# Kernel optimization log

Hardware: AMD Instinct MI355X
Metric: run time of the kernel (lower is better)

## Reference

```python
import jax, jax.numpy as jnp
import numpy as np

H, HS, NH, T = 2048, 64, 32, 1024
DD, DA, DG, DV = 64, 64, 128, 32


def _ln(x, w, b, eps):
    mu = x.mean(-1, keepdims=True)
    var = ((x - mu) ** 2).mean(-1, keepdims=True)
    return (x - mu) / jnp.sqrt(var + eps) * w + b


def setup_inputs() -> dict:
    key = jax.random.key(0)
    ks = jax.random.split(key, 40)
    n = lambda i, shape, s=0.02: (jax.random.normal(ks[i], shape, jnp.float32) * s)
    u = lambda i, shape: jax.random.uniform(ks[i], shape, jnp.float32)
    return {
        'x': jax.random.normal(ks[0], (1, T, H), jnp.float32),
        'state1': jax.random.normal(ks[1], (1, H), jnp.float32),
        'state2': jnp.zeros((NH, HS, HS), jnp.float32),
        'v_first': jax.random.normal(ks[2], (1, T, H), jnp.float32),
        'x_r': u(3, (H,)), 'x_w': u(4, (H,)), 'x_k': u(5, (H,)),
        'x_v': u(6, (H,)), 'x_a': u(7, (H,)), 'x_g': u(8, (H,)),
        'W_r': n(9, (H, H)), 'W_k': n(10, (H, H)), 'W_v': n(11, (H, H)), 'W_o': n(12, (H, H)),
        'w0': n(13, (H,), 0.5) - 0.6,
        'w1': n(14, (H, DD)), 'w2': n(15, (DD, H)),
        'a0': jnp.zeros((H,), jnp.float32), 'a1': n(16, (H, DA)), 'a2': n(17, (DA, H)),
        'v0': jnp.zeros((H,), jnp.float32), 'v1': n(18, (H, DV)), 'v2': n(19, (DV, H)),
        'g1': n(20, (H, DG)), 'g2': n(21, (DG, H)),
        'k_k': n(22, (NH, HS), 0.5) + 1.0, 'k_a': n(23, (NH, HS), 0.5) + 1.0,
        'r_k': n(24, (NH, HS), 0.5),
        'ln_x_w': jnp.ones((H,), jnp.float32), 'ln_x_b': jnp.zeros((H,), jnp.float32),
        'ln1_w': jnp.ones((H,), jnp.float32), 'ln1_b': jnp.zeros((H,), jnp.float32),
    }


def reference(x, state1, state2, v_first, x_r, x_w, x_k, x_v, x_a, x_g,
              W_r, W_k, W_v, W_o, w0, w1, w2, a0, a1, a2, v0, v1, v2,
              g1, g2, k_k, k_a, r_k, ln_x_w, ln_x_b, ln1_w, ln1_b):
    T = x.shape[1]
    NH, HS = k_k.shape
    Hd = NH * HS
    last_x = x
    xn = _ln(x, ln1_w, ln1_b, 1e-5)
    # token shift: sx = shifted_past - x
    past = jnp.concatenate([state1[:, None, :], xn[:, :-1, :]], axis=1)
    sx = past - xn
    state1_out = xn[:, -1, :]
    xr = xn + x_r * sx
    xw = xn + x_w * sx
    xk = xn + x_k * sx
    xv = xn + x_v * sx
    xa = xn + x_a * sx
    xg = xn + x_g * sx
    r = xr @ W_r.T                                  # [1,T,H]
    k = (xk @ W_k.T).reshape(T, NH, HS)
    v = xv @ W_v.T                                  # [1,T,H]
    g = jax.nn.sigmoid(xg @ g1) @ g2                # gate
    a = jax.nn.sigmoid(a0 + (xa @ a1) @ a2).reshape(T, NH, HS)
    w = jnp.tanh(xw @ w1) @ w2                      # decay LoRA
    kk = k * k_k
    kk = kk / (jnp.linalg.norm(kk, axis=-1, keepdims=True) + 1e-12)
    k = k * (1.0 + (a - 1.0) * k_a)
    # layer_id != 0: v residual toward v_first
    v = v + (v_first - v) * jax.nn.sigmoid(v0 + (xv @ v1) @ v2)
    w = jnp.exp(-0.606531 * jax.nn.sigmoid(w0 + w)).reshape(T, NH, HS)
    b_seq = kk * a        # in-context addition direction
    a_seq = -kk           # removal direction
    r3 = r.reshape(T, NH, HS)
    v3 = v.reshape(T, NH, HS)

    def step(S, ts):
        w_t, k_t, v_t, a_t, b_t, r_t = ts          # each [NH,HS]
        S = S * w_t[:, None, :]                     # column-wise decay
        sa = jnp.einsum('hij,hj->hi', S, a_t)       # S @ a
        S = S + sa[:, :, None] * b_t[:, None, :] + v_t[:, :, None] * k_t[:, None, :]
        out = jnp.einsum('hij,hj->hi', S, r_t)      # S @ r
        return S, out

    state2_out, y = jax.lax.scan(step, state2, (w, k, v3, a_seq, b_seq, r3))  # y: [T,NH,HS]
    y = _ln(y, 1.0, 0.0, 0.00064)                   # GroupNorm-style per-head LN (no affine)
    y = y.reshape(1, T, Hd) * ln_x_w + ln_x_b
    bonus = ((r3 * k * r_k).sum(-1, keepdims=True) * v3).reshape(1, T, Hd)
    y = (y + bonus) * g
    y = y @ W_o.T
    return (last_x + y, state1_out, state2_out, v_first)
```

## Files before the change

### kernel.cpp

```cpp
#include <hip/hip_runtime.h>
#include <hip/hip_bf16.h>
#include <cstdint>
#include <cstddef>

#define T_TOK 1024
#define H_DIM 2048
#define NH 32
#define HS 64
#define TH (T_TOK * H_DIM)
#define HH (H_DIM * H_DIM)

using short8 = __attribute__((ext_vector_type(8))) short;
using f32x4  = __attribute__((ext_vector_type(4))) float;
typedef __hip_bfloat16 bf16;

__device__ __forceinline__ float sigmoidf_(float x) { return 1.0f / (1.0f + expf(-x)); }

__device__ __forceinline__ float wsum64(float v) {
#pragma unroll
    for (int m = 32; m; m >>= 1) v += __shfl_xor(v, m, 64);
    return v;
}

__device__ __forceinline__ float dpp_add16(float x) {
    int t;
    t = __builtin_amdgcn_update_dpp(0, __float_as_int(x), 0xB1, 0xF, 0xF, true);
    x += __int_as_float(t);
    t = __builtin_amdgcn_update_dpp(0, __float_as_int(x), 0x4E, 0xF, 0xF, true);
    x += __int_as_float(t);
    t = __builtin_amdgcn_update_dpp(0, __float_as_int(x), 0x141, 0xF, 0xF, true);
    x += __int_as_float(t);
    t = __builtin_amdgcn_update_dpp(0, __float_as_int(x), 0x140, 0xF, 0xF, true);
    x += __int_as_float(t);
    return x;
}

struct CastPar { const float* src[4]; bf16* dst[4]; };
__global__ __launch_bounds__(256) void castw_kernel(CastPar p) {
    int z = blockIdx.z;
    const float4* s = (const float4*)p.src[z];
    bf16* d = p.dst[z];
    int i = blockIdx.x * 256 + threadIdx.x;
    float4 v = s[i];
    int b = i * 4;
    d[b + 0] = __float2bfloat16(v.x);
    d[b + 1] = __float2bfloat16(v.y);
    d[b + 2] = __float2bfloat16(v.z);
    d[b + 3] = __float2bfloat16(v.w);
}

struct TPar { const float* src[8]; bf16* dst[8]; int R[8]; int C[8]; };
__global__ __launch_bounds__(256) void transpose_kernel(TPar p) {
    int z = blockIdx.z;
    int R = p.R[z], C = p.C[z];
    int e = blockIdx.x * 256 + threadIdx.x;
    if (e >= R * C) return;
    int r = e / C, c = e % C;
    p.dst[z][(size_t)c * R + r] = __float2bfloat16(p.src[z][e]);
}

__global__ __launch_bounds__(256) void ln_kernel(const float* __restrict__ x,
                                                 const float* __restrict__ w,
                                                 const float* __restrict__ b,
                                                 float* __restrict__ xn,
                                                 float* __restrict__ s1out) {
    int t = blockIdx.x, tid = threadIdx.x;
    const float* xt = x + (size_t)t * H_DIM;
    float v[8]; float s = 0.f, s2 = 0.f;
#pragma unroll
    for (int e = 0; e < 8; e++) { v[e] = xt[tid + 256 * e]; s += v[e]; s2 += v[e] * v[e]; }
    s = wsum64(s); s2 = wsum64(s2);
    __shared__ float ls[8];
    int wid = tid >> 6, ln = tid & 63;
    if (ln == 0) { ls[wid] = s; ls[4 + wid] = s2; }
    __syncthreads();
    s = ls[0] + ls[1] + ls[2] + ls[3];
    s2 = ls[4] + ls[5] + ls[6] + ls[7];
    float mu = s * (1.f / H_DIM);
    float var = s2 * (1.f / H_DIM) - mu * mu;
    float inv = rsqrtf(var + 1e-5f);
#pragma unroll
    for (int e = 0; e < 8; e++) {
        int h = tid + 256 * e;
        float o = (v[e] - mu) * inv * w[h] + b[h];
        xn[(size_t)t * H_DIM + h] = o;
        if (t == T_TOK - 1) s1out[h] = o;
    }
}

struct MixPar { const float* xn; const float* state1; const float* mv[6]; bf16* out[6]; };
__global__ __launch_bounds__(256) void mix_kernel(MixPar p) {
    int t = blockIdx.x, tid = threadIdx.x;
#pragma unroll
    for (int e = 0; e < 8; e++) {
        int h = tid + 256 * e;
        size_t idx = (size_t)t * H_DIM + h;
        float cur = p.xn[idx];
        float prev = (t == 0) ? p.state1[h] : p.xn[idx - H_DIM];
        float sx = prev - cur;
#pragma unroll
        for (int q = 0; q < 6; q++)
            p.out[q][idx] = __float2bfloat16(cur + p.mv[q][h] * sx);
    }
}

typedef const __attribute__((address_space(1))) uint32_t* gp1_t;
typedef __attribute__((address_space(3))) uint32_t* lp3_t;
__device__ __forceinline__ void async16(const bf16* g, short* l) {
    __builtin_amdgcn_global_load_lds((gp1_t)g, (lp3_t)l, 16, 0, 0);
}

struct BGPar { const bf16* X[4]; const bf16* W[4]; float* out[4]; const float* resid[4]; };
__global__ __launch_bounds__(256) void bgemm_kernel(BGPar p) {
    int z = blockIdx.z;
    const bf16* __restrict__ X = p.X[z];
    const bf16* __restrict__ W = p.W[z];
    float* __restrict__ out = p.out[z];
    const float* __restrict__ resid = p.resid[z];

    __shared__ short As[4][128 * 32];
    __shared__ short Bs[4][128 * 32];

    int m0 = blockIdx.y * 128, n0 = blockIdx.x * 128;
    int tid = threadIdx.x, lane = tid & 63, wv = tid >> 6;
    int m_off = (wv >> 1) * 64, n_off = (wv & 1) * 64;
    int lr = lane & 15, lq = lane >> 4;

    int srow = lane >> 2;
    int scol = (lane & 3) * 8;
    const bf16* Ag0 = X + (size_t)(m0 + wv * 32 + srow) * 2048 + scol;
    const bf16* Ag1 = Ag0 + (size_t)16 * 2048;
    const bf16* Bg0 = W + (size_t)(n0 + wv * 32 + srow) * 2048 + scol;
    const bf16* Bg1 = Bg0 + (size_t)16 * 2048;

    auto issue = [&](int at, int nb) {
        int kk = at * 32;
        async16(Ag0 + kk, &As[nb][(wv * 32) * 32]);
        async16(Ag1 + kk, &As[nb][(wv * 32 + 16) * 32]);
        async16(Bg0 + kk, &Bs[nb][(wv * 32) * 32]);
        async16(Bg1 + kk, &Bs[nb][(wv * 32 + 16) * 32]);
    };

    f32x4 acc[4][4];
#pragma unroll
    for (int a = 0; a < 4; a++)
#pragma unroll
        for (int b = 0; b < 4; b++)
#pragma unroll
            for (int r = 0; r < 4; r++) acc[a][b][r] = 0.f;

    issue(0, 0); issue(1, 1); issue(2, 2);

    for (int it = 0; it < 64; it++) {
        int nt = it + 3;
        int at = nt > 63 ? 63 : nt;
        issue(at, nt & 3);
        asm volatile("s_waitcnt vmcnt(12)" ::: "memory");
        asm volatile("s_barrier" ::: "memory");
        int buf = it & 3;
        short8 af[4], bfr[4];
#pragma unroll
        for (int mi = 0; mi < 4; mi++)
            af[mi] = *(const short8*)&As[buf][(m_off + mi * 16 + lr) * 32 + lq * 8];
#pragma unroll
        for (int ni = 0; ni < 4; ni++)
            bfr[ni] = *(const short8*)&Bs[buf][(n_off + ni * 16 + lr) * 32 + lq * 8];
#pragma unroll
        for (int mi = 0; mi < 4; mi++)
#pragma unroll
            for (int ni = 0; ni < 4; ni++)
                acc[mi][ni] = __builtin_amdgcn_mfma_f32_16x16x32_bf16(af[mi], bfr[ni], acc[mi][ni], 0, 0, 0);
        asm volatile("s_barrier" ::: "memory");
    }
    asm volatile("s_waitcnt vmcnt(0)" ::: "memory");

#pragma unroll
    for (int mi = 0; mi < 4; mi++)
#pragma unroll
        for (int ni = 0; ni < 4; ni++)
#pragma unroll
            for (int r = 0; r < 4; r++) {
                int rowg = m0 + m_off + mi * 16 + lq * 4 + r;
                int colg = n0 + n_off + ni * 16 + lr;
                size_t o = (size_t)rowg * 2048 + colg;
                float v = acc[mi][ni][r];
                if (resid) v += resid[o];
                out[o] = v;
            }
}

#define BM 128
#define BN 128
#define BK 32
#define LDK 40

__device__ __forceinline__ void gemm_core(const bf16* __restrict__ X, const bf16* __restrict__ W,
                                          int M, int N, int K, int act,
                                          const float* __restrict__ bias,
                                          float* __restrict__ outF, bf16* __restrict__ outB) {
    __shared__ short As[BM * LDK];
    __shared__ short Bs[BN * LDK];
    int m0 = blockIdx.y * BM, n0 = blockIdx.x * BN;
    if (n0 >= N) return;
    int tid = threadIdx.x;
    int lane = tid & 63, wid = tid >> 6;
    int m_off = (wid >> 1) * 64, n_off = (wid & 1) * 64;
    int lr = lane & 15, lq = lane >> 4;

    f32x4 acc[4][4];
#pragma unroll
    for (int a = 0; a < 4; a++)
#pragma unroll
        for (int b = 0; b < 4; b++)
#pragma unroll
            for (int r = 0; r < 4; r++) acc[a][b][r] = 0.f;

    for (int k0 = 0; k0 < K; k0 += BK) {
#pragma unroll
        for (int it = 0; it < 2; it++) {
            int c = tid + it * 256;
            int r = c >> 2;
            int cc = (c & 3) * 8;
            uint4 va = *(const uint4*)(X + (size_t)(m0 + r) * K + k0 + cc);
            *(uint4*)&As[r * LDK + cc] = va;
            uint4 vb;
            if (n0 + r < N) vb = *(const uint4*)(W + (size_t)(n0 + r) * K + k0 + cc);
            else            vb = make_uint4(0u, 0u, 0u, 0u);
            *(uint4*)&Bs[r * LDK + cc] = vb;
        }
        __syncthreads();
        short8 af[4], bfr[4];
#pragma unroll
        for (int mi = 0; mi < 4; mi++)
            af[mi] = *(const short8*)&As[(m_off + mi * 16 + lr) * LDK + lq * 8];
#pragma unroll
        for (int ni = 0; ni < 4; ni++)
            bfr[ni] = *(const short8*)&Bs[(n_off + ni * 16 + lr) * LDK + lq * 8];
#pragma unroll
        for (int mi = 0; mi < 4; mi++)
#pragma unroll
            for (int ni = 0; ni < 4; ni++)
                acc[mi][ni] = __builtin_amdgcn_mfma_f32_16x16x32_bf16(af[mi], bfr[ni], acc[mi][ni], 0, 0, 0);
        __syncthreads();
    }
#pragma unroll
    for (int mi = 0; mi < 4; mi++)
#pragma unroll
        for (int ni = 0; ni < 4; ni++)
#pragma unroll
            for (int r = 0; r < 4; r++) {
                int rowg = m0 + m_off + mi * 16 + lq * 4 + r;
                int colg = n0 + n_off + ni * 16 + lr;
                if (colg < N) {
                    float v = acc[mi][ni][r];
                    if (bias) v += bias[colg];
                    if (act == 1) v = sigmoidf_(v);
                    else if (act == 2) v = tanhf(v);
                    size_t o = (size_t)rowg * N + colg;
                    if (outF) outF[o] = v;
                    else      outB[o] = __float2bfloat16(v);
                }
            }
}

struct GPar {
    const bf16* X[4]; const bf16* W[4];
    float* outF[4]; bf16* outB[4];
    const float* bias[4];
    int N[4]; int K[4]; int act[4]; int M;
};
__global__ __launch_bounds__(256) void gemm_z_kernel(GPar p) {
    int z = blockIdx.z;
    gemm_core(p.X[z], p.W[z], p.M, p.N[z], p.K[z], p.act[z], p.bias[z], p.outF[z], p.outB[z]);
}

__global__ __launch_bounds__(64) void prep_kernel(float* __restrict__ k_io, float* __restrict__ v_io,
                                                  const float* __restrict__ v_first,
                                                  const float* __restrict__ vres,
                                                  float* __restrict__ w_io, float* __restrict__ a_io,
                                                  float* __restrict__ as_out,
                                                  const float* __restrict__ k_k,
                                                  const float* __restrict__ k_a,
                                                  const float* __restrict__ w0) {
    int h = blockIdx.x, t = blockIdx.y, i = threadIdx.x;
    int hi = h * HS + i;
    size_t idx = (size_t)t * H_DIM + hi;
    float kf = k_io[idx];
    float kk = kf * k_k[hi];
    float ss = wsum64(kk * kk);
    float kkn = kk / (sqrtf(ss) + 1e-12f);
    float a = a_io[idx];
    k_io[idx] = kf * (1.f + (a - 1.f) * k_a[hi]);
    float vv = v_io[idx];
    v_io[idx] = vv + (v_first[idx] - vv) * vres[idx];
    w_io[idx] = expf(-0.606531f * sigmoidf_(w0[hi] + w_io[idx]));
    a_io[idx] = kkn * a;
    as_out[idx] = -kkn;
}

struct SlotV { f32x4 w, a, b, k, r; float v; };

#define SCAN_ISSUE(sl, tt)                                                              \
    do {                                                                                \
        int tc_ = (tt) < T_TOK ? (tt) : T_TOK - 1;                                      \
        const float* wp_ = w_s + (size_t)tc_ * H_DIM + hb;                              \
        const float* ap_ = as_s + (size_t)tc_ * H_DIM + hb;                             \
        const float* bp_ = b_s + (size_t)tc_ * H_DIM + hb;                              \
        const float* kp_ = k_s + (size_t)tc_ * H_DIM + hb;                              \
        const float* rp_ = r_s + (size_t)tc_ * H_DIM + hb;                              \
        const float* vp_ = v_s + (size_t)tc_ * H_DIM + hb;                              \
        asm volatile("global_load_dwordx4 %0, %1, %2" : "=v"((sl).w) : "v"(jow), "s"(wp_)); \
        asm volatile("global_load_dwordx4 %0, %1, %2" : "=v"((sl).a) : "v"(jow), "s"(ap_)); \
        asm volatile("global_load_dwordx4 %0, %1, %2" : "=v"((sl).b) : "v"(jow), "s"(bp_)); \
        asm volatile("global_load_dwordx4 %0, %1, %2" : "=v"((sl).k) : "v"(jow), "s"(kp_)); \
        asm volatile("global_load_dwordx4 %0, %1, %2" : "=v"((sl).r) : "v"(jow), "s"(rp_)); \
        asm volatile("global_load_dword %0, %1, %2" : "=v"((sl).v) : "v"(rowoff), "s"(vp_)); \
    } while (0)

#define SCAN_PIN(sl)                                                                    \
    asm volatile("" : "+v"((sl).w), "+v"((sl).a), "+v"((sl).b), "+v"((sl).k),           \
                      "+v"((sl).r), "+v"((sl).v))

__device__ __forceinline__ void scan_compute(float S[4], const SlotV& s,
                                             const float* __restrict__ yp, int rowoff) {
    float sa = 0.f;
#pragma unroll
    for (int e = 0; e < 4; e++) { S[e] *= s.w[e]; sa = fmaf(S[e], s.a[e], sa); }
    sa = dpp_add16(sa);
    float o = 0.f;
#pragma unroll
    for (int e = 0; e < 4; e++) {
        S[e] = fmaf(sa, s.b[e], fmaf(s.v, s.k[e], S[e]));
        o = fmaf(S[e], s.r[e], o);
    }
    o = dpp_add16(o);
    asm volatile("global_store_dword %0, %1, %2" :: "v"(rowoff), "v"(o), "s"(yp) : "memory");
}

#define SCAN_STEP(d, t, W)                                                              \
    do {                                                                                \
        asm volatile("s_waitcnt vmcnt(" W ")");                                         \
        SCAN_PIN(sv[d]);                                                                \
        scan_compute(S, sv[d], y + (size_t)(t) * H_DIM + hb, rowoff);                   \
        SCAN_ISSUE(sv[d], (t) + 4);                                                     \
    } while (0)

__global__ __launch_bounds__(64) void scan_kernel(const float* __restrict__ w_s,
                                                  const float* __restrict__ k_s,
                                                  const float* __restrict__ v_s,
                                                  const float* __restrict__ as_s,
                                                  const float* __restrict__ b_s,
                                                  const float* __restrict__ r_s,
                                                  const float* __restrict__ s2in,
                                                  float* __restrict__ y,
                                                  float* __restrict__ s2out) {
    int h = blockIdx.x, q = blockIdx.y;
    int lane = threadIdx.x;
    int il = lane >> 4, jb = lane & 15;
    int row = q * 4 + il;
    int jo = jb * 4;
    int hb = h * HS;
    int jow = jo * 4;
    int rowoff = row * 4;

    float S[4];
    {
        const float* s0 = s2in + (size_t)h * HS * HS + (size_t)row * HS + jo;
        float4 t0 = *(const float4*)s0;
        S[0] = t0.x; S[1] = t0.y; S[2] = t0.z; S[3] = t0.w;
    }

    SlotV sv[4];
    SCAN_ISSUE(sv[0], 0);
    SCAN_ISSUE(sv[1], 1);
    SCAN_ISSUE(sv[2], 2);
    SCAN_ISSUE(sv[3], 3);

    SCAN_STEP(0, 0, "18");
    SCAN_STEP(1, 1, "19");
    SCAN_STEP(2, 2, "20");
    SCAN_STEP(3, 3, "21");
    for (int tb = 4; tb < T_TOK; tb += 4) {
        SCAN_STEP(0, tb + 0, "21");
        SCAN_STEP(1, tb + 1, "21");
        SCAN_STEP(2, tb + 2, "21");
        SCAN_STEP(3, tb + 3, "21");
    }
    asm volatile("s_waitcnt vmcnt(0)" ::: "memory");

    {
        float* so = s2out + (size_t)h * HS * HS + (size_t)row * HS + jo;
        float4 t0;
        t0.x = S[0]; t0.y = S[1]; t0.z = S[2]; t0.w = S[3];
        *(float4*)so = t0;
    }
}

__global__ __launch_bounds__(64) void post_kernel(const float* __restrict__ y,
                                                  const float* __restrict__ r_s,
                                                  const float* __restrict__ k_s,
                                                  const float* __restrict__ v_s,
                                                  const float* __restrict__ g_s,
                                                  const float* __restrict__ r_k,
                                                  const float* __restrict__ lnw,
                                                  const float* __restrict__ lnb,
                                                  bf16* __restrict__ ybig) {
    int h = blockIdx.x, t = blockIdx.y, i = threadIdx.x;
    int hi = h * HS + i;
    size_t idx = (size_t)t * H_DIM + hi;
    float yv = y[idx];
    float mu = wsum64(yv) * (1.f / HS);
    float d = yv - mu;
    float var = wsum64(d * d) * (1.f / HS);
    float yn = d * rsqrtf(var + 0.00064f);
    float bd = wsum64(r_s[idx] * k_s[idx] * r_k[hi]);
    float val = (yn * lnw[hi] + lnb[hi] + bd * v_s[idx]) * g_s[idx];
    ybig[idx] = __float2bfloat16(val);
}

extern "C" void kernel_launch(void* const* d_in, const int* in_sizes, int n_in,
                              void* d_out, int out_size, void* d_ws, size_t ws_size,
                              hipStream_t stream) {
    const float* x      = (const float*)d_in[0];
    const float* state1 = (const float*)d_in[1];
    const float* state2 = (const float*)d_in[2];
    const float* vfirst = (const float*)d_in[3];
    const float* x_r = (const float*)d_in[4];
    const float* x_w = (const float*)d_in[5];
    const float* x_k = (const float*)d_in[6];
    const float* x_v = (const float*)d_in[7];
    const float* x_a = (const float*)d_in[8];
    const float* x_g = (const float*)d_in[9];
    const float* W_r = (const float*)d_in[10];
    const float* W_k = (const float*)d_in[11];
    const float* W_v = (const float*)d_in[12];
    const float* W_o = (const float*)d_in[13];
    const float* w0 = (const float*)d_in[14];
    const float* w1 = (const float*)d_in[15];
    const float* w2 = (const float*)d_in[16];
    const float* a0 = (const float*)d_in[17];
    const float* a1 = (const float*)d_in[18];
    const float* a2 = (const float*)d_in[19];
    const float* v0 = (const float*)d_in[20];
    const float* v1 = (const float*)d_in[21];
    const float* v2 = (const float*)d_in[22];
    const float* g1 = (const float*)d_in[23];
    const float* g2 = (const float*)d_in[24];
    const float* k_k = (const float*)d_in[25];
    const float* k_a = (const float*)d_in[26];
    const float* r_k = (const float*)d_in[27];
    const float* ln_x_w = (const float*)d_in[28];
    const float* ln_x_b = (const float*)d_in[29];
    const float* ln1_w = (const float*)d_in[30];
    const float* ln1_b = (const float*)d_in[31];

    float* out0 = (float*)d_out;
    float* out1 = out0 + TH;
    float* out2 = out1 + H_DIM;
    float* out3 = out2 + NH * HS * HS;

    float* F = (float*)d_ws;
    float* xn   = F;
    float* as_s = F;
    float* rb   = F + (size_t)1 * TH;
    float* kb   = F + (size_t)2 * TH;
    float* vb   = F + (size_t)3 * TH;
    float* ab   = F + (size_t)4 * TH;
    float* wpre = F + (size_t)5 * TH;
    float* vresb= F + (size_t)6 * TH;
    float* gb   = F + (size_t)7 * TH;
    float* yb   = F + (size_t)8 * TH;
    bf16* B = (bf16*)(F + (size_t)9 * TH);
    bf16 *xrb = B, *xwb = B + (size_t)TH, *xkb = B + (size_t)2 * TH,
         *xvb = B + (size_t)3 * TH, *xab = B + (size_t)4 * TH, *xgb = B + (size_t)5 * TH;
    bf16* Wrb = B + (size_t)6 * TH;
    bf16* Wkb = Wrb + (size_t)HH;
    bf16* Wvb = Wkb + (size_t)HH;
    bf16* Wob = Wvb + (size_t)HH;
    bf16* pp = Wob + (size_t)HH;
    bf16* a1T = pp; pp += (size_t)H_DIM * 64;
    bf16* w1T = pp; pp += (size_t)H_DIM * 64;
    bf16* v1T = pp; pp += (size_t)H_DIM * 32;
    bf16* g1T = pp; pp += (size_t)H_DIM * 128;
    bf16* a2T = pp; pp += (size_t)H_DIM * 64;
    bf16* w2T = pp; pp += (size_t)H_DIM * 64;
    bf16* v2T = pp; pp += (size_t)H_DIM * 32;
    bf16* g2T = pp; pp += (size_t)H_DIM * 128;
    bf16* amid = pp; pp += (size_t)T_TOK * 64;
    bf16* wmid = pp; pp += (size_t)T_TOK * 64;
    bf16* vmid = pp; pp += (size_t)T_TOK * 32;
    bf16* gmid = pp; pp += (size_t)T_TOK * 128;
    bf16* ybig = pp; pp += (size_t)TH;

    CastPar cp;
    cp.src[0] = W_r; cp.src[1] = W_k; cp.src[2] = W_v; cp.src[3] = W_o;
    cp.dst[0] = Wrb; cp.dst[1] = Wkb; cp.dst[2] = Wvb; cp.dst[3] = Wob;
    castw_kernel<<<dim3(HH / 4 / 256, 1, 4), 256, 0, stream>>>(cp);

    TPar tp;
    tp.src[0] = a1; tp.dst[0] = a1T; tp.R[0] = H_DIM; tp.C[0] = 64;
    tp.src[1] = w1; tp.dst[1] = w1T; tp.R[1] = H_DIM; tp.C[1] = 64;
    tp.src[2] = v1; tp.dst[2] = v1T; tp.R[2] = H_DIM; tp.C[2] = 32;
    tp.src[3] = g1; tp.dst[3] = g1T; tp.R[3] = H_DIM; tp.C[3] = 128;
    tp.src[4] = a2; tp.dst[4] = a2T; tp.R[4] = 64;  tp.C[4] = H_DIM;
    tp.src[5] = w2; tp.dst[5] = w2T; tp.R[5] = 64;  tp.C[5] = H_DIM;
    tp.src[6] = v2; tp.dst[6] = v2T; tp.R[6] = 32;  tp.C[6] = H_DIM;
    tp.src[7] = g2; tp.dst[7] = g2T; tp.R[7] = 128; tp.C[7] = H_DIM;
    transpose_kernel<<<dim3((H_DIM * 128 + 255) / 256, 1, 8), 256, 0, stream>>>(tp);

    ln_kernel<<<dim3(T_TOK), 256, 0, stream>>>(x, ln1_w, ln1_b, xn, out1);

    MixPar mp; mp.xn = xn; mp.state1 = state1;
    mp.mv[0] = x_r; mp.mv[1] = x_w; mp.mv[2] = x_k; mp.mv[3] = x_v; mp.mv[4] = x_a; mp.mv[5] = x_g;
    mp.out[0] = xrb; mp.out[1] = xwb; mp.out[2] = xkb; mp.out[3] = xvb; mp.out[4] = xab; mp.out[5] = xgb;
    mix_kernel<<<dim3(T_TOK), 256, 0, stream>>>(mp);

    BGPar bp{};
    bp.X[0] = xrb; bp.W[0] = Wrb; bp.out[0] = rb; bp.resid[0] = nullptr;
    bp.X[1] = xkb; bp.W[1] = Wkb; bp.out[1] = kb; bp.resid[1] = nullptr;
    bp.X[2] = xvb; bp.W[2] = Wvb; bp.out[2] = vb; bp.resid[2] = nullptr;
    bgemm_kernel<<<dim3(16, 8, 3), 256, 0, stream>>>(bp);

    GPar s1{}; s1.M = T_TOK;
    s1.X[0] = xab; s1.W[0] = a1T; s1.outB[0] = amid; s1.N[0] = 64;  s1.K[0] = H_DIM; s1.act[0] = 0;
    s1.X[1] = xwb; s1.W[1] = w1T; s1.outB[1] = wmid; s1.N[1] = 64;  s1.K[1] = H_DIM; s1.act[1] = 2;
    s1.X[2] = xvb; s1.W[2] = v1T; s1.outB[2] = vmid; s1.N[2] = 32;  s1.K[2] = H_DIM; s1.act[2] = 0;
    s1.X[3] = xgb; s1.W[3] = g1T; s1.outB[3] = gmid; s1.N[3] = 128; s1.K[3] = H_DIM; s1.act[3] = 1;
    gemm_z_kernel<<<dim3(1, 8, 4), 256, 0, stream>>>(s1);

    GPar s2{}; s2.M = T_TOK;
    s2.X[0] = amid; s2.W[0] = a2T; s2.outF[0] = ab;    s2.N[0] = H_DIM; s2.K[0] = 64;  s2.act[0] = 1; s2.bias[0] = a0;
    s2.X[1] = wmid; s2.W[1] = w2T; s2.outF[1] = wpre;  s2.N[1] = H_DIM; s2.K[1] = 64;  s2.act[1] = 0;
    s2.X[2] = vmid; s2.W[2] = v2T; s2.outF[2] = vresb; s2.N[2] = H_DIM; s2.K[2] = 32;  s2.act[2] = 1; s2.bias[2] = v0;
    s2.X[3] = gmid; s2.W[3] = g2T; s2.outF[3] = gb;    s2.N[3] = H_DIM; s2.K[3] = 128; s2.act[3] = 0;
    gemm_z_kernel<<<dim3(16, 8, 4), 256, 0, stream>>>(s2);

    prep_kernel<<<dim3(NH, T_TOK), 64, 0, stream>>>(kb, vb, vfirst, vresb, wpre, ab, as_s, k_k, k_a, w0);

    scan_kernel<<<dim3(NH, 16), 64, 0, stream>>>(wpre, kb, vb, as_s, ab, rb, state2, yb, out2);

    post_kernel<<<dim3(NH, T_TOK), 64, 0, stream>>>(yb, rb, kb, vb, gb, r_k, ln_x_w, ln_x_b, ybig);

    BGPar bo{};
    bo.X[0] = ybig; bo.W[0] = Wob; bo.out[0] = out0; bo.resid[0] = x;
    bgemm_kernel<<<dim3(16, 8, 1), 256, 0, stream>>>(bo);

    hipMemcpyAsync(out3, (const void*)vfirst, (size_t)TH * sizeof(float),
                   hipMemcpyDeviceToDevice, stream);
}
```

Measured before the change: 577.8 us.

## Pack scan inputs a, b, k, r as interleaved bf16 to cut scan loads

The prep kernel now writes the removal direction, addition direction, new k and r as bf16 into one packed per-token, per-head buffer. The buffer is interleaved so each scan lane fetches all four 4-element groups with two 16-byte loads instead of four fp32 16-byte loads. This cuts the memory traffic and load count in the latency-bound sequential scan, and the vmcnt wait thresholds are adjusted to match. The cost is bf16 precision in the recurrent state update, which could push error across 1024 steps. The packed buffer reuses the W_r bf16 cast region, which is no longer needed at that point.

```diff
diff --git a/kernel.cpp b/kernel.cpp
--- a/kernel.cpp
+++ b/kernel.cpp
@@ -12,6 +12,7 @@
 
 using short8 = __attribute__((ext_vector_type(8))) short;
 using f32x4  = __attribute__((ext_vector_type(4))) float;
+using i32x4  = __attribute__((ext_vector_type(4))) int;
 typedef __hip_bfloat16 bf16;
 
 __device__ __forceinline__ float sigmoidf_(float x) { return 1.0f / (1.0f + expf(-x)); }
@@ -277,8 +278,10 @@
 __global__ __launch_bounds__(64) void prep_kernel(float* __restrict__ k_io, float* __restrict__ v_io,
                                                   const float* __restrict__ v_first,
                                                   const float* __restrict__ vres,
-                                                  float* __restrict__ w_io, float* __restrict__ a_io,
-                                                  float* __restrict__ as_out,
+                                                  float* __restrict__ w_io,
+                                                  const float* __restrict__ a_io,
+                                                  const float* __restrict__ r_in,
+                                                  bf16* __restrict__ pk,
                                                   const float* __restrict__ k_k,
                                                   const float* __restrict__ k_a,
                                                   const float* __restrict__ w0) {
@@ -290,48 +293,56 @@
     float ss = wsum64(kk * kk);
     float kkn = kk / (sqrtf(ss) + 1e-12f);
     float a = a_io[idx];
-    k_io[idx] = kf * (1.f + (a - 1.f) * k_a[hi]);
+    float knew = kf * (1.f + (a - 1.f) * k_a[hi]);
+    k_io[idx] = knew;
     float vv = v_io[idx];
     v_io[idx] = vv + (v_first[idx] - vv) * vres[idx];
     w_io[idx] = expf(-0.606531f * sigmoidf_(w0[hi] + w_io[idx]));
-    a_io[idx] = kkn * a;
-    as_out[idx] = -kkn;
-}
-
-struct SlotV { f32x4 w, a, b, k, r; float v; };
+    size_t pb = (((size_t)t * NH + h) * 16 + (i >> 2)) * 16 + (i & 3);
+    pk[pb + 0]  = __float2bfloat16(-kkn);
+    pk[pb + 4]  = __float2bfloat16(kkn * a);
+    pk[pb + 8]  = __float2bfloat16(knew);
+    pk[pb + 12] = __float2bfloat16(r_in[idx]);
+}
+
+struct SlotV { f32x4 w; i32x4 q0, q1; float v; };
 
 #define SCAN_ISSUE(sl, tt)                                                              \
     do {                                                                                \
         int tc_ = (tt) < T_TOK ? (tt) : T_TOK - 1;                                      \
         const float* wp_ = w_s + (size_t)tc_ * H_DIM + hb;                              \
-        const float* ap_ = as_s + (size_t)tc_ * H_DIM + hb;                             \
-        const float* bp_ = b_s + (size_t)tc_ * H_DIM + hb;                              \
-        const float* kp_ = k_s + (size_t)tc_ * H_DIM + hb;                              \
-        const float* rp_ = r_s + (size_t)tc_ * H_DIM + hb;                              \
+        const bf16*  pp_ = pk + (size_t)tc_ * (NH * 256) + h * 256;                     \
         const float* vp_ = v_s + (size_t)tc_ * H_DIM + hb;                              \
         asm volatile("global_load_dwordx4 %0, %1, %2" : "=v"((sl).w) : "v"(jow), "s"(wp_)); \
-        asm volatile("global_load_dwordx4 %0, %1, %2" : "=v"((sl).a) : "v"(jow), "s"(ap_)); \
-        asm volatile("global_load_dwordx4 %0, %1, %2" : "=v"((sl).b) : "v"(jow), "s"(bp_)); \
-        asm volatile("global_load_dwordx4 %0, %1, %2" : "=v"((sl).k) : "v"(jow), "s"(kp_)); \
-        asm volatile("global_load_dwordx4 %0, %1, %2" : "=v"((sl).r) : "v"(jow), "s"(rp_)); \
+        asm volatile("global_load_dwordx4 %0, %1, %2" : "=v"((sl).q0) : "v"(pko), "s"(pp_)); \
+        asm volatile("global_load_dwordx4 %0, %1, %2 offset:16" : "=v"((sl).q1) : "v"(pko), "s"(pp_)); \
         asm volatile("global_load_dword %0, %1, %2" : "=v"((sl).v) : "v"(rowoff), "s"(vp_)); \
     } while (0)
 
 #define SCAN_PIN(sl)                                                                    \
-    asm volatile("" : "+v"((sl).w), "+v"((sl).a), "+v"((sl).b), "+v"((sl).k),           \
-                      "+v"((sl).r), "+v"((sl).v))
+    asm volatile("" : "+v"((sl).w), "+v"((sl).q0), "+v"((sl).q1), "+v"((sl).v))
 
 __device__ __forceinline__ void scan_compute(float S[4], const SlotV& s,
                                              const float* __restrict__ yp, int rowoff) {
+    float af[4], bb[4], kf[4], rf[4];
+    uint32_t u;
+    u = (uint32_t)s.q0[0]; af[0] = __uint_as_float(u << 16); af[1] = __uint_as_float(u & 0xffff0000u);
+    u = (uint32_t)s.q0[1]; af[2] = __uint_as_float(u << 16); af[3] = __uint_as_float(u & 0xffff0000u);
+    u = (uint32_t)s.q0[2]; bb[0] = __uint_as_float(u << 16); bb[1] = __uint_as_float(u & 0xffff0000u);
+    u = (uint32_t)s.q0[3]; bb[2] = __uint_as_float(u << 16); bb[3] = __uint_as_float(u & 0xffff0000u);
+    u = (uint32_t)s.q1[0]; kf[0] = __uint_as_float(u << 16); kf[1] = __uint_as_float(u & 0xffff0000u);
+    u = (uint32_t)s.q1[1]; kf[2] = __uint_as_float(u << 16); kf[3] = __uint_as_float(u & 0xffff0000u);
+    u = (uint32_t)s.q1[2]; rf[0] = __uint_as_float(u << 16); rf[1] = __uint_as_float(u & 0xffff0000u);
+    u = (uint32_t)s.q1[3]; rf[2] = __uint_as_float(u << 16); rf[3] = __uint_as_float(u & 0xffff0000u);
     float sa = 0.f;
 #pragma unroll
-    for (int e = 0; e < 4; e++) { S[e] *= s.w[e]; sa = fmaf(S[e], s.a[e], sa); }
+    for (int e = 0; e < 4; e++) { S[e] *= s.w[e]; sa = fmaf(S[e], af[e], sa); }
     sa = dpp_add16(sa);
     float o = 0.f;
 #pragma unroll
     for (int e = 0; e < 4; e++) {
-        S[e] = fmaf(sa, s.b[e], fmaf(s.v, s.k[e], S[e]));
-        o = fmaf(S[e], s.r[e], o);
+        S[e] = fmaf(sa, bb[e], fmaf(s.v, kf[e], S[e]));
+        o = fmaf(S[e], rf[e], o);
     }
     o = dpp_add16(o);
     asm volatile("global_store_dword %0, %1, %2" :: "v"(rowoff), "v"(o), "s"(yp) : "memory");
@@ -346,11 +357,8 @@
     } while (0)
 
 __global__ __launch_bounds__(64) void scan_kernel(const float* __restrict__ w_s,
-                                                  const float* __restrict__ k_s,
+                                                  const bf16* __restrict__ pk,
                                                   const float* __restrict__ v_s,
-                                                  const float* __restrict__ as_s,
-                                                  const float* __restrict__ b_s,
-                                                  const float* __restrict__ r_s,
                                                   const float* __restrict__ s2in,
                                                   float* __restrict__ y,
                                                   float* __restrict__ s2out) {
@@ -361,6 +369,7 @@
     int jo = jb * 4;
     int hb = h * HS;
     int jow = jo * 4;
+    int pko = jb * 32;
     int rowoff = row * 4;
 
     float S[4];
@@ -376,15 +385,15 @@
     SCAN_ISSUE(sv[2], 2);
     SCAN_ISSUE(sv[3], 3);
 
-    SCAN_STEP(0, 0, "18");
-    SCAN_STEP(1, 1, "19");
-    SCAN_STEP(2, 2, "20");
-    SCAN_STEP(3, 3, "21");
+    SCAN_STEP(0, 0, "12");
+    SCAN_STEP(1, 1, "13");
+    SCAN_STEP(2, 2, "14");
+    SCAN_STEP(3, 3, "15");
     for (int tb = 4; tb < T_TOK; tb += 4) {
-        SCAN_STEP(0, tb + 0, "21");
-        SCAN_STEP(1, tb + 1, "21");
-        SCAN_STEP(2, tb + 2, "21");
-        SCAN_STEP(3, tb + 3, "21");
+        SCAN_STEP(0, tb + 0, "15");
+        SCAN_STEP(1, tb + 1, "15");
+        SCAN_STEP(2, tb + 2, "15");
+        SCAN_STEP(3, tb + 3, "15");
     }
     asm volatile("s_waitcnt vmcnt(0)" ::: "memory");
 
@@ -461,7 +470,6 @@
 
     float* F = (float*)d_ws;
     float* xn   = F;
-    float* as_s = F;
     float* rb   = F + (size_t)1 * TH;
     float* kb   = F + (size_t)2 * TH;
     float* vb   = F + (size_t)3 * TH;
@@ -492,6 +500,8 @@
     bf16* gmid = pp; pp += (size_t)T_TOK * 128;
     bf16* ybig = pp; pp += (size_t)TH;
 
+    bf16* PK = Wrb;
+
     CastPar cp;
     cp.src[0] = W_r; cp.src[1] = W_k; cp.src[2] = W_v; cp.src[3] = W_o;
     cp.dst[0] = Wrb; cp.dst[1] = Wkb; cp.dst[2] = Wvb; cp.dst[3] = Wob;
@@ -535,9 +545,9 @@
     s2.X[3] = gmid; s2.W[3] = g2T; s2.outF[3] = gb;    s2.N[3] = H_DIM; s2.K[3] = 128; s2.act[3] = 0;
     gemm_z_kernel<<<dim3(16, 8, 4), 256, 0, stream>>>(s2);
 
-    prep_kernel<<<dim3(NH, T_TOK), 64, 0, stream>>>(kb, vb, vfirst, vresb, wpre, ab, as_s, k_k, k_a, w0);
-
-    scan_kernel<<<dim3(NH, 16), 64, 0, stream>>>(wpre, kb, vb, as_s, ab, rb, state2, yb, out2);
+    prep_kernel<<<dim3(NH, T_TOK), 64, 0, stream>>>(kb, vb, vfirst, vresb, wpre, ab, rb, PK, k_k, k_a, w0);
+
+    scan_kernel<<<dim3(NH, 16), 64, 0, stream>>>(wpre, PK, vb, state2, yb, out2);
 
     post_kernel<<<dim3(NH, T_TOK), 64, 0, stream>>>(yb, rb, kb, vb, gb, r_k, ln_x_w, ln_x_b, ybig);
 
```

Result: slower. 593.6 us (+2.7%).
